# Kernel tuning notes

Hardware: AMD Instinct MI355X
Metric: run time of the kernel (lower is better)

The kernel has to match this reference:

```python
import jax, jax.numpy as jnp
import numpy as np

KH, KW = 3, 3
STRIDE = (1, 1)
PADDING = (1, 1)
DILATION = (1, 1)


def setup_inputs() -> dict:
    key = jax.random.key(0)
    k1, k2, k3, k4, k5 = jax.random.split(key, 5)
    B, Cin, H, W = 8, 64, 128, 128
    Cout = 64
    Ho, Wo = 128, 128  # stride 1, pad 1, k=3 -> same spatial size
    K = KH * KW
    return {
        "input": jax.random.normal(k1, (B, Cin, H, W), dtype=jnp.float32),
        "offset": jax.random.normal(k2, (B, 2 * K, Ho, Wo), dtype=jnp.float32),
        "mask": jax.random.uniform(k3, (B, K, Ho, Wo), dtype=jnp.float32),
        "weight": jax.random.normal(k4, (Cout, Cin, KH, KW), dtype=jnp.float32) * 0.05,
        "bias": jax.random.normal(k5, (Cout,), dtype=jnp.float32) * 0.05,
    }


def _deform_conv2d(x, weight, offset, mask, bias, stride, padding, dilation):
    B, Cin, H, W = x.shape
    Cout, Cing, kh, kw = weight.shape
    G = Cin // Cing                      # weight groups
    K = kh * kw
    Goff = offset.shape[1] // (2 * K)    # offset groups
    Ho, Wo = offset.shape[2], offset.shape[3]
    Cg = Cin // Goff                     # channels per offset group
    sh, sw = stride
    ph, pw = padding
    dh, dw = dilation

    # offsets laid out as (y, x) pairs per kernel tap per offset group
    off = offset.reshape(B, Goff, K, 2, Ho, Wo)
    ky = (jnp.arange(K) // kw).astype(jnp.float32) * dh   # [K]
    kx = (jnp.arange(K) % kw).astype(jnp.float32) * dw
    gy = (jnp.arange(Ho).astype(jnp.float32) * sh - ph)    # [Ho]
    gx = (jnp.arange(Wo).astype(jnp.float32) * sw - pw)
    # sampling positions: [B, Goff, K, Ho, Wo]
    py = off[:, :, :, 0] + ky[None, None, :, None, None] + gy[None, None, None, :, None]
    px = off[:, :, :, 1] + kx[None, None, :, None, None] + gx[None, None, None, None, :]

    y0 = jnp.floor(py)
    x0 = jnp.floor(px)
    ly = py - y0
    lx = px - x0
    y0i = y0.astype(jnp.int32)
    x0i = x0.astype(jnp.int32)

    x_g = x.reshape(B, Goff, Cg, H * W)

    def gather(yi, xi):
        # zero padding outside the image
        valid = (yi >= 0) & (yi < H) & (xi >= 0) & (xi < W)
        yc = jnp.clip(yi, 0, H - 1)
        xc = jnp.clip(xi, 0, W - 1)
        idx = (yc * W + xc).reshape(B, Goff, K * Ho * Wo)
        v = jnp.take_along_axis(x_g, idx[:, :, None, :], axis=3)  # [B,Goff,Cg,K*Ho*Wo]
        return v * valid.reshape(B, Goff, 1, K * Ho * Wo)

    w00 = ((1 - ly) * (1 - lx)).reshape(B, Goff, 1, K * Ho * Wo)
    w01 = ((1 - ly) * lx).reshape(B, Goff, 1, K * Ho * Wo)
    w10 = (ly * (1 - lx)).reshape(B, Goff, 1, K * Ho * Wo)
    w11 = (ly * lx).reshape(B, Goff, 1, K * Ho * Wo)

    sampled = w00 * gather(y0i, x0i)
    sampled = sampled + w01 * gather(y0i, x0i + 1)
    sampled = sampled + w10 * gather(y0i + 1, x0i)
    sampled = sampled + w11 * gather(y0i + 1, x0i + 1)
    sampled = sampled.reshape(B, Goff, Cg, K, Ho, Wo)

    if mask is not None:
        sampled = sampled * mask.reshape(B, Goff, 1, K, Ho, Wo)

    # grouped conv accumulate
    sampled = sampled.reshape(B, G, Cing, K, Ho, Wo)
    w = weight.reshape(G, Cout // G, Cing, K)
    out = jnp.einsum('gock,bgcksq->bgosq', w, sampled).reshape(B, Cout, Ho, Wo)
    if bias is not None:
        out = out + bias[None, :, None, None]
    return out


def reference(input, offset, mask, weight, bias):
    return _deform_conv2d(input, weight, offset, mask, bias, STRIDE, PADDING, DILATION)
```

## Files before the change

kernel.cpp:

```cpp
#include <hip/hip_runtime.h>
#include <hip/hip_fp16.h>

#define HH 128
#define WW 128
#define HW (HH*WW)
#define XT_BYTES ((size_t)8 * HW * 64 * 2)
#define WT_BYTES ((size_t)9 * 2 * 4 * 64 * 8 * 2)

typedef __attribute__((ext_vector_type(8))) short short8;
typedef __attribute__((ext_vector_type(4))) float f32x4;

static __device__ __forceinline__ unsigned short f2bf(float f) {
    unsigned int u = __float_as_uint(f);
    u += 0x7fffu + ((u >> 16) & 1u);
    return (unsigned short)(u >> 16);
}
static __device__ __forceinline__ float bf2f(unsigned short h) {
    return __uint_as_float((unsigned int)h << 16);
}
static __device__ __forceinline__ float blo(unsigned int u) {
    return __uint_as_float(u << 16);
}
static __device__ __forceinline__ float bhi(unsigned int u) {
    return __uint_as_float(u & 0xffff0000u);
}

__global__ void wtrans_kernel(const float* __restrict__ w, unsigned short* __restrict__ wt) {
    int i = blockIdx.x * 256 + threadIdx.x;
    if (i < 9 * 2 * 4 * 64 * 8) {
        int e  = i & 7;
        int l  = (i >> 3) & 63;
        int wv = (i >> 9) & 3;
        int kf = (i >> 11) & 1;
        int k  = i >> 12;
        int co = wv * 16 + (l & 15);
        int c  = kf * 32 + (l >> 4) * 8 + e;
        wt[i] = f2bf(w[(co * 64 + c) * 9 + k]);
    }
}

__global__ __launch_bounds__(256) void xtrans_kernel(const float* __restrict__ x,
                                                     unsigned int* __restrict__ xt32) {
    __shared__ float tile[64][65];
    const int bid = blockIdx.x;
    const int b   = bid >> 8;
    const int hw0 = (bid & 255) << 6;
    const int t   = threadIdx.x;
    #pragma unroll
    for (int i = 0; i < 16; ++i) {
        int idx = (i << 8) + t;
        int c = idx >> 6, j = idx & 63;
        tile[c][j] = x[(size_t)(((b << 6) + c) << 14) + hw0 + j];
    }
    __syncthreads();
    #pragma unroll
    for (int i = 0; i < 8; ++i) {
        int idx = (i << 8) + t;
        int cp = idx & 31, hw = idx >> 5;
        unsigned u = (unsigned)f2bf(tile[2 * cp][hw]) | ((unsigned)f2bf(tile[2 * cp + 1][hw]) << 16);
        xt32[((size_t)((b << 14) + hw0 + hw) << 5) + cp] = u;
    }
}

__global__ __launch_bounds__(256, 5) void deform_nhwc(
    const unsigned short* __restrict__ xt,
    const float* __restrict__ off,
    const float* __restrict__ msk,
    const unsigned short* __restrict__ wt,
    const float* __restrict__ bias,
    float* __restrict__ out)
{
    __shared__ __align__(16) unsigned char smem[30208];
    int4*  moS = (int4*)(smem + 16384);
    uint2* mwH = (uint2*)(smem + 25600);

    const int t   = threadIdx.x;
    const int bid = blockIdx.x;
    const int b   = bid & 7;
    const int rem = bid >> 3;
    const int ho  = rem >> 1;
    const int wo0 = (rem & 1) << 6;
    const int l   = t & 63;
    const int wv_id = __builtin_amdgcn_readfirstlane(t >> 6);

    short8 wtf[2][2];
    #pragma unroll
    for (int kf = 0; kf < 2; ++kf)
        wtf[0][kf] = *(const short8*)(wt + (((kf * 4 + wv_id) * 64 + l) << 3));

    for (int i = t; i < 9 * 64; i += 256) {
        int p = i & 63;
        int k = i >> 6;
        int wo = wo0 + p;
        int obase = ((b * 18 + 2 * k) * HH + ho) * WW + wo;
        float oy = off[obase];
        float ox = off[obase + HW];
        float m  = msk[((b * 9 + k) * HH + ho) * WW + wo];
        float py = oy + (float)(k / 3) + (float)(ho - 1);
        float px = ox + (float)(k % 3) + (float)(wo - 1);
        float fy = floorf(py), fx = floorf(px);
        float ly = py - fy,    lx = px - fx;
        int y0 = (int)fy, x0 = (int)fx;
        int y1 = y0 + 1,  x1 = x0 + 1;
        float vy0 = (y0 >= 0 && y0 < HH) ? 1.f : 0.f;
        float vy1 = (y1 >= 0 && y1 < HH) ? 1.f : 0.f;
        float vx0 = (x0 >= 0 && x0 < WW) ? 1.f : 0.f;
        float vx1 = (x1 >= 0 && x1 < WW) ? 1.f : 0.f;
        float w00 = (1.f - ly) * (1.f - lx) * m * vy0 * vx0;
        float w01 = (1.f - ly) * lx         * m * vy0 * vx1;
        float w10 = ly         * (1.f - lx) * m * vy1 * vx0;
        float w11 = ly         * lx         * m * vy1 * vx1;
        int yc0 = min(max(y0, 0), HH - 1), yc1 = min(max(y1, 0), HH - 1);
        int xc0 = min(max(x0, 0), WW - 1), xc1 = min(max(x1, 0), WW - 1);
        moS[i] = make_int4((yc0 * WW + xc0) << 7, (yc0 * WW + xc1) << 7,
                           (yc1 * WW + xc0) << 7, (yc1 * WW + xc1) << 7);
        __half2 hA = __floats2half2_rn(w00, w01);
        __half2 hB = __floats2half2_rn(w10, w11);
        mwH[i] = make_uint2(*(unsigned int*)&hA, *(unsigned int*)&hB);
    }

    const char* ib = (const char*)xt + (size_t)b * HW * 128;
    const int chb  = (l & 7) << 4;
    const int px0_ = (wv_id << 4) + (l >> 3);
    int st_woff[2];
    st_woff[0] = px0_ * 128 + (chb ^ ((px0_ & 7) << 4));
    st_woff[1] = st_woff[0] + 8 * 128;
    const int lq = (l >> 4) << 4;
    const int sw = (l & 7) << 4;

    __syncthreads();

    auto sample_tap = [&](int k, unsigned char* dst) {
        #pragma unroll
        for (int r = 0; r < 2; ++r) {
            const int px = px0_ + (r << 3);
            int4   ob = moS[k * 64 + px];
            uint2  wp = mwH[k * 64 + px];
            float2 wA = __half22float2(*(const __half2*)&wp.x);
            float2 wB = __half22float2(*(const __half2*)&wp.y);
            uint4 c00 = *(const uint4*)(ib + (ob.x + chb));
            uint4 c01 = *(const uint4*)(ib + (ob.y + chb));
            uint4 c10 = *(const uint4*)(ib + (ob.z + chb));
            uint4 c11 = *(const uint4*)(ib + (ob.w + chb));
            uint4 uv;
            #define CMB(dst_, a0, a1, a2, a3) {                                         \
                float vlo = wA.x*blo(a0) + wA.y*blo(a1) + wB.x*blo(a2) + wB.y*blo(a3);  \
                float vhi = wA.x*bhi(a0) + wA.y*bhi(a1) + wB.x*bhi(a2) + wB.y*bhi(a3);  \
                dst_ = __builtin_amdgcn_perm(__float_as_uint(vhi) + 0x8000u,            \
                                             __float_as_uint(vlo) + 0x8000u, 0x07060302u); }
            CMB(uv.x, c00.x, c01.x, c10.x, c11.x);
            CMB(uv.y, c00.y, c01.y, c10.y, c11.y);
            CMB(uv.z, c00.z, c01.z, c10.z, c11.z);
            CMB(uv.w, c00.w, c01.w, c10.w, c11.w);
            #undef CMB
            *(uint4*)(dst + st_woff[r]) = uv;
        }
    };

    sample_tap(0, smem);
    __syncthreads();

    f32x4 acc[4];
    #pragma unroll
    for (int g = 0; g < 4; ++g) acc[g] = (f32x4){0.f, 0.f, 0.f, 0.f};

    #pragma unroll
    for (int s = 0; s < 9; ++s) {
        if (s < 8) {
            const int kn = s + 1;
            #pragma unroll
            for (int kf = 0; kf < 2; ++kf)
                wtf[kn & 1][kf] = *(const short8*)(wt + ((((kn * 2 + kf) * 4 + wv_id) * 64 + l) << 3));
            sample_tap(kn, smem + ((kn & 1) << 13));
        }
        const unsigned char* rb = smem + ((s & 1) << 13);
        #pragma unroll
        for (int g = 0; g < 4; ++g) {
            const int prow = g * 16 + (l & 15);
            short8 a0 = *(const short8*)(rb + prow * 128 + (lq ^ sw));
            short8 a1 = *(const short8*)(rb + prow * 128 + ((64 + lq) ^ sw));
            acc[g] = __builtin_amdgcn_mfma_f32_16x16x32_bf16(a0, wtf[s & 1][0], acc[g], 0, 0, 0);
            acc[g] = __builtin_amdgcn_mfma_f32_16x16x32_bf16(a1, wtf[s & 1][1], acc[g], 0, 0, 0);
        }
        __syncthreads();
    }

    float* out_t = (float*)smem;
    const int co_e = (wv_id << 4) + (l & 15);
    const float bv = bias[co_e];
    const int swE = (co_e & 15) << 4;
    #pragma unroll
    for (int g = 0; g < 4; ++g) {
        int pxb = (g << 6) + ((l >> 4) << 4);
        float4 v = make_float4(acc[g][0] + bv, acc[g][1] + bv, acc[g][2] + bv, acc[g][3] + bv);
        *(float4*)((unsigned char*)out_t + co_e * 256 + (pxb ^ swE)) = v;
    }
    __syncthreads();
    float* outb = out + (size_t)b * 64 * HW + (size_t)ho * WW + wo0;
    #pragma unroll
    for (int j = 0; j < 4; ++j) {
        int co   = (t >> 4) + (j << 4);
        int colb = (t & 15) << 4;
        float4 v = *(const float4*)((const unsigned char*)out_t + co * 256 + (colb ^ ((co & 15) << 4)));
        *(float4*)&outb[(size_t)co * HW + ((t & 15) << 2)] = v;
    }
}

__global__ __launch_bounds__(256, 4) void deform_fallback(
    const float* __restrict__ x, const float* __restrict__ off,
    const float* __restrict__ msk, const float* __restrict__ wraw,
    const float* __restrict__ bias, float* __restrict__ out)
{
    __shared__ unsigned short s_tile[2][64][68];
    __shared__ __align__(16) unsigned char meta_mem[18432];
    float4* mwS = (float4*)meta_mem;
    int4*   moS = (int4*)(meta_mem + 9216);
    float*  out_t = (float*)meta_mem;

    const int t   = threadIdx.x;
    const int bid = blockIdx.x;
    const int b   = bid & 7;
    const int rem = bid >> 3;
    const int ho  = rem >> 1;
    const int wo0 = (rem & 1) << 6;
    const int l   = t & 63;
    const int wv_id = __builtin_amdgcn_readfirstlane(t >> 6);
    const int c0  = wv_id << 4;
    const int cb  = wv_id << 4;

    short8 wtf[2][2];
    #pragma unroll
    for (int kf = 0; kf < 2; ++kf) {
        short8 f;
        int co = cb + (l & 15);
        int cbase = kf * 32 + (l >> 4) * 8;
        #pragma unroll
        for (int e = 0; e < 8; ++e) f[e] = (short)f2bf(wraw[(co * 64 + cbase + e) * 9 + 0]);
        wtf[0][kf] = f;
    }

    for (int i = t; i < 9 * 64; i += 256) {
        int p = i & 63;
        int k = i >> 6;
        int wo = wo0 + p;
        int obase = ((b * 18 + 2 * k) * HH + ho) * WW + wo;
        float oy = off[obase];
        float ox = off[obase + HW];
        float m  = msk[((b * 9 + k) * HH + ho) * WW + wo];
        float py = oy + (float)(k / 3) + (float)(ho - 1);
        float px = ox + (float)(k % 3) + (float)(wo - 1);
        float fy = floorf(py), fx = floorf(px);
        float ly = py - fy,    lx = px - fx;
        int y0 = (int)fy, x0 = (int)fx;
        int y1 = y0 + 1,  x1 = x0 + 1;
        float vy0 = (y0 >= 0 && y0 < HH) ? 1.f : 0.f;
        float vy1 = (y1 >= 0 && y1 < HH) ? 1.f : 0.f;
        float vx0 = (x0 >= 0 && x0 < WW) ? 1.f : 0.f;
        float vx1 = (x1 >= 0 && x1 < WW) ? 1.f : 0.f;
        float w00 = (1.f - ly) * (1.f - lx) * m * vy0 * vx0;
        float w01 = (1.f - ly) * lx         * m * vy0 * vx1;
        float w10 = ly         * (1.f - lx) * m * vy1 * vx0;
        float w11 = ly         * lx         * m * vy1 * vx1;
        int yc0 = min(max(y0, 0), HH - 1), yc1 = min(max(y1, 0), HH - 1);
        int xc0 = min(max(x0, 0), WW - 1), xc1 = min(max(x1, 0), WW - 1);
        mwS[i] = make_float4(w00, w01, w10, w11);
        moS[i] = make_int4(yc0 * WW + xc0, yc0 * WW + xc1,
                           yc1 * WW + xc0, yc1 * WW + xc1);
    }

    const int p = t & 63;
    const float* xb = x + (size_t)(b * 64 + c0) * HW;
    __syncthreads();

    {
        float4 wv = mwS[p];
        int4   ov = moS[p];
        const float* pc = xb;
        #pragma unroll
        for (int i = 0; i < 16; i += 4) {
            float v0 = wv.x * pc[ov.x] + wv.y * pc[ov.y] + wv.z * pc[ov.z] + wv.w * pc[ov.w]; pc += HW;
            float v1 = wv.x * pc[ov.x] + wv.y * pc[ov.y] + wv.z * pc[ov.z] + wv.w * pc[ov.w]; pc += HW;
            float v2 = wv.x * pc[ov.x] + wv.y * pc[ov.y] + wv.z * pc[ov.z] + wv.w * pc[ov.w]; pc += HW;
            float v3 = wv.x * pc[ov.x] + wv.y * pc[ov.y] + wv.z * pc[ov.z] + wv.w * pc[ov.w]; pc += HW;
            uint2 u;
            u.x = (unsigned)f2bf(v0) | ((unsigned)f2bf(v1) << 16);
            u.y = (unsigned)f2bf(v2) | ((unsigned)f2bf(v3) << 16);
            *(uint2*)&s_tile[0][p][c0 + i] = u;
        }
    }
    __syncthreads();

    f32x4 acc[4];
    #pragma unroll
    for (int g = 0; g < 4; ++g) acc[g] = (f32x4){0.f, 0.f, 0.f, 0.f};

    #pragma unroll
    for (int s = 0; s < 9; ++s) {
        if (s < 8) {
            const int kn = s + 1;
            #pragma unroll
            for (int kf = 0; kf < 2; ++kf) {
                short8 f;
                int co = cb + (l & 15);
                int cbase = kf * 32 + (l >> 4) * 8;
                #pragma unroll
                for (int e = 0; e < 8; ++e) f[e] = (short)f2bf(wraw[(co * 64 + cbase + e) * 9 + kn]);
                wtf[kn & 1][kf] = f;
            }
            float4 wv = mwS[kn * 64 + p];
            int4   ov = moS[kn * 64 + p];
            const float* pc = xb;
            #pragma unroll
            for (int i = 0; i < 16; i += 4) {
                float v0 = wv.x * pc[ov.x] + wv.y * pc[ov.y] + wv.z * pc[ov.z] + wv.w * pc[ov.w]; pc += HW;
                float v1 = wv.x * pc[ov.x] + wv.y * pc[ov.y] + wv.z * pc[ov.z] + wv.w * pc[ov.w]; pc += HW;
                float v2 = wv.x * pc[ov.x] + wv.y * pc[ov.y] + wv.z * pc[ov.z] + wv.w * pc[ov.w]; pc += HW;
                float v3 = wv.x * pc[ov.x] + wv.y * pc[ov.y] + wv.z * pc[ov.z] + wv.w * pc[ov.w]; pc += HW;
                uint2 u;
                u.x = (unsigned)f2bf(v0) | ((unsigned)f2bf(v1) << 16);
                u.y = (unsigned)f2bf(v2) | ((unsigned)f2bf(v3) << 16);
                *(uint2*)&s_tile[kn & 1][p][c0 + i] = u;
            }
        }
        #pragma unroll
        for (int g = 0; g < 4; ++g) {
            const int prow = g * 16 + (l & 15);
            const unsigned short* rp = &s_tile[s & 1][prow][(l >> 4) * 8];
            union { short8 v; unsigned long long q[2]; } ua0, ua1;
            ua0.q[0] = *(const unsigned long long*)(rp);
            ua0.q[1] = *(const unsigned long long*)(rp + 4);
            ua1.q[0] = *(const unsigned long long*)(rp + 32);
            ua1.q[1] = *(const unsigned long long*)(rp + 36);
            acc[g] = __builtin_amdgcn_mfma_f32_16x16x32_bf16(ua0.v, wtf[s & 1][0], acc[g], 0, 0, 0);
            acc[g] = __builtin_amdgcn_mfma_f32_16x16x32_bf16(ua1.v, wtf[s & 1][1], acc[g], 0, 0, 0);
        }
        __syncthreads();
    }

    const float bv = bias[cb + (l & 15)];
    #pragma unroll
    for (int g = 0; g < 4; ++g) {
        int co = cb + (l & 15);
        int pxb = g * 16 + (l >> 4) * 4;
        #pragma unroll
        for (int r = 0; r < 4; ++r)
            out_t[co * 68 + pxb + r] = acc[g][r] + bv;
    }
    __syncthreads();
    float* outb = out + (size_t)b * 64 * HW + (size_t)ho * WW + wo0;
    #pragma unroll
    for (int j = 0; j < 4; ++j) {
        int co  = (t >> 4) + j * 16;
        int px0 = (t & 15) << 2;
        float4 v = *(float4*)&out_t[co * 68 + px0];
        *(float4*)&outb[(size_t)co * HW + px0] = v;
    }
}

extern "C" void kernel_launch(void* const* d_in, const int* in_sizes, int n_in,
                              void* d_out, int out_size, void* d_ws, size_t ws_size,
                              hipStream_t stream) {
    const float* x    = (const float*)d_in[0];
    const float* off  = (const float*)d_in[1];
    const float* msk  = (const float*)d_in[2];
    const float* w    = (const float*)d_in[3];
    const float* bias = (const float*)d_in[4];
    float* out = (float*)d_out;

    const size_t need = XT_BYTES + WT_BYTES;
    if (d_ws != nullptr && ws_size >= need) {
        unsigned int*   xt32 = (unsigned int*)d_ws;
        unsigned short* wt   = (unsigned short*)((char*)d_ws + XT_BYTES);
        xtrans_kernel<<<2048, 256, 0, stream>>>(x, xt32);
        wtrans_kernel<<<144, 256, 0, stream>>>(w, wt);
        deform_nhwc<<<2048, 256, 0, stream>>>((const unsigned short*)xt32, off, msk, wt, bias, out);
    } else {
        deform_fallback<<<2048, 256, 0, stream>>>(x, off, msk, w, bias, out);
    }
}
```

Before: 52.73 us.

## Feed bilinear samples straight into MFMA registers, dropping LDS staging and barriers

Restructures the main loop so each wave samples its own 16 pixels across all 64 channels and builds MFMA A-fragments directly in registers, instead of writing sampled taps to LDS and reading them back. Gathers for the next tap are issued into a double-buffered register set while the current tap is combined, and the per-tap __syncthreads is removed. Each wave now computes all 64 output channels, so it loads 8 weight fragments per tap. Occupancy is lowered to 3 blocks per SM to make room for the larger register footprint, which may reduce the latency hiding available for the gathers.

```diff
diff --git a/kernel.cpp b/kernel.cpp
--- a/kernel.cpp
+++ b/kernel.cpp
@@ -14,9 +14,6 @@
     unsigned int u = __float_as_uint(f);
     u += 0x7fffu + ((u >> 16) & 1u);
     return (unsigned short)(u >> 16);
-}
-static __device__ __forceinline__ float bf2f(unsigned short h) {
-    return __uint_as_float((unsigned int)h << 16);
 }
 static __device__ __forceinline__ float blo(unsigned int u) {
     return __uint_as_float(u << 16);
@@ -62,7 +59,7 @@
     }
 }
 
-__global__ __launch_bounds__(256, 5) void deform_nhwc(
+__global__ __launch_bounds__(256, 3) void deform_nhwc(
     const unsigned short* __restrict__ xt,
     const float* __restrict__ off,
     const float* __restrict__ msk,
@@ -81,12 +78,7 @@
     const int ho  = rem >> 1;
     const int wo0 = (rem & 1) << 6;
     const int l   = t & 63;
-    const int wv_id = __builtin_amdgcn_readfirstlane(t >> 6);
-
-    short8 wtf[2][2];
-    #pragma unroll
-    for (int kf = 0; kf < 2; ++kf)
-        wtf[0][kf] = *(const short8*)(wt + (((kf * 4 + wv_id) * 64 + l) << 3));
+    const int wv  = __builtin_amdgcn_readfirstlane(t >> 6);
 
     for (int i = t; i < 9 * 64; i += 256) {
         int p = i & 63;
@@ -119,80 +111,85 @@
         mwH[i] = make_uint2(*(unsigned int*)&hA, *(unsigned int*)&hB);
     }
 
-    const char* ib = (const char*)xt + (size_t)b * HW * 128;
-    const int chb  = (l & 7) << 4;
-    const int px0_ = (wv_id << 4) + (l >> 3);
-    int st_woff[2];
-    st_woff[0] = px0_ * 128 + (chb ^ ((px0_ & 7) << 4));
-    st_woff[1] = st_woff[0] + 8 * 128;
-    const int lq = (l >> 4) << 4;
-    const int sw = (l & 7) << 4;
-
-    __syncthreads();
-
-    auto sample_tap = [&](int k, unsigned char* dst) {
-        #pragma unroll
-        for (int r = 0; r < 2; ++r) {
-            const int px = px0_ + (r << 3);
-            int4   ob = moS[k * 64 + px];
-            uint2  wp = mwH[k * 64 + px];
-            float2 wA = __half22float2(*(const __half2*)&wp.x);
-            float2 wB = __half22float2(*(const __half2*)&wp.y);
-            uint4 c00 = *(const uint4*)(ib + (ob.x + chb));
-            uint4 c01 = *(const uint4*)(ib + (ob.y + chb));
-            uint4 c10 = *(const uint4*)(ib + (ob.z + chb));
-            uint4 c11 = *(const uint4*)(ib + (ob.w + chb));
-            uint4 uv;
-            #define CMB(dst_, a0, a1, a2, a3) {                                         \
-                float vlo = wA.x*blo(a0) + wA.y*blo(a1) + wB.x*blo(a2) + wB.y*blo(a3);  \
-                float vhi = wA.x*bhi(a0) + wA.y*bhi(a1) + wB.x*bhi(a2) + wB.y*bhi(a3);  \
-                dst_ = __builtin_amdgcn_perm(__float_as_uint(vhi) + 0x8000u,            \
-                                             __float_as_uint(vlo) + 0x8000u, 0x07060302u); }
-            CMB(uv.x, c00.x, c01.x, c10.x, c11.x);
-            CMB(uv.y, c00.y, c01.y, c10.y, c11.y);
-            CMB(uv.z, c00.z, c01.z, c10.z, c11.z);
-            CMB(uv.w, c00.w, c01.w, c10.w, c11.w);
-            #undef CMB
-            *(uint4*)(dst + st_woff[r]) = uv;
+    const char* ib  = (const char*)xt + (size_t)b * HW * 128;
+    const int   px  = (wv << 4) + (l & 15);
+    const int   chb = (l >> 4) << 4;
+
+    __syncthreads();
+
+    f32x4 acc[4];
+    #pragma unroll
+    for (int g = 0; g < 4; ++g) acc[g] = (f32x4){0.f, 0.f, 0.f, 0.f};
+
+    uint4 ga[8], gb[8];
+
+    #define ISSUE_G(g, kk) {                                                \
+        int4 ob = moS[(kk) * 64 + px];                                      \
+        g[0] = *(const uint4*)(ib + ob.x + chb);                            \
+        g[1] = *(const uint4*)(ib + ob.x + chb + 64);                       \
+        g[2] = *(const uint4*)(ib + ob.y + chb);                            \
+        g[3] = *(const uint4*)(ib + ob.y + chb + 64);                       \
+        g[4] = *(const uint4*)(ib + ob.z + chb);                            \
+        g[5] = *(const uint4*)(ib + ob.z + chb + 64);                       \
+        g[6] = *(const uint4*)(ib + ob.w + chb);                            \
+        g[7] = *(const uint4*)(ib + ob.w + chb + 64);                       \
+    }
+
+    #define CMB(dst_, a0, a1, a2, a3) {                                     \
+        float vlo = wA.x*blo(a0) + wA.y*blo(a1) + wB.x*blo(a2) + wB.y*blo(a3); \
+        float vhi = wA.x*bhi(a0) + wA.y*bhi(a1) + wB.x*bhi(a2) + wB.y*bhi(a3); \
+        dst_ = __builtin_amdgcn_perm(__float_as_uint(vhi) + 0x8000u,        \
+                                     __float_as_uint(vlo) + 0x8000u, 0x07060302u); }
+
+    #define COMBINE_MFMA(g, kk, bfr) {                                      \
+        uint2 wp = mwH[(kk) * 64 + px];                                     \
+        float2 wA = __half22float2(*(const __half2*)&wp.x);                 \
+        float2 wB = __half22float2(*(const __half2*)&wp.y);                 \
+        short8 af[2];                                                       \
+        _Pragma("unroll")                                                   \
+        for (int kf = 0; kf < 2; ++kf) {                                    \
+            uint4 c00 = g[0 + kf], c01 = g[2 + kf], c10 = g[4 + kf], c11 = g[6 + kf]; \
+            unsigned r0, r1, r2, r3;                                        \
+            CMB(r0, c00.x, c01.x, c10.x, c11.x);                            \
+            CMB(r1, c00.y, c01.y, c10.y, c11.y);                            \
+            CMB(r2, c00.z, c01.z, c10.z, c11.z);                            \
+            CMB(r3, c00.w, c01.w, c10.w, c11.w);                            \
+            union { unsigned u[4]; short8 s; } uu = {{r0, r1, r2, r3}};     \
+            af[kf] = uu.s;                                                  \
+        }                                                                   \
+        _Pragma("unroll")                                                   \
+        for (int cot = 0; cot < 4; ++cot) {                                 \
+            acc[cot] = __builtin_amdgcn_mfma_f32_16x16x32_bf16(af[0], bfr[cot],     acc[cot], 0, 0, 0); \
+            acc[cot] = __builtin_amdgcn_mfma_f32_16x16x32_bf16(af[1], bfr[4 + cot], acc[cot], 0, 0, 0); \
+        }                                                                   \
+    }
+
+    ISSUE_G(ga, 0)
+
+    #pragma unroll
+    for (int k = 0; k < 9; ++k) {
+        short8 bfr[8];
+        #pragma unroll
+        for (int q = 0; q < 8; ++q)
+            bfr[q] = *(const short8*)(wt + (((k * 8 + q) * 64 + l) << 3));
+        if (k < 8) {
+            if (k & 1) { ISSUE_G(ga, k + 1) } else { ISSUE_G(gb, k + 1) }
         }
-    };
-
-    sample_tap(0, smem);
-    __syncthreads();
-
-    f32x4 acc[4];
-    #pragma unroll
-    for (int g = 0; g < 4; ++g) acc[g] = (f32x4){0.f, 0.f, 0.f, 0.f};
-
-    #pragma unroll
-    for (int s = 0; s < 9; ++s) {
-        if (s < 8) {
-            const int kn = s + 1;
-            #pragma unroll
-            for (int kf = 0; kf < 2; ++kf)
-                wtf[kn & 1][kf] = *(const short8*)(wt + ((((kn * 2 + kf) * 4 + wv_id) * 64 + l) << 3));
-            sample_tap(kn, smem + ((kn & 1) << 13));
-        }
-        const unsigned char* rb = smem + ((s & 1) << 13);
-        #pragma unroll
-        for (int g = 0; g < 4; ++g) {
-            const int prow = g * 16 + (l & 15);
-            short8 a0 = *(const short8*)(rb + prow * 128 + (lq ^ sw));
-            short8 a1 = *(const short8*)(rb + prow * 128 + ((64 + lq) ^ sw));
-            acc[g] = __builtin_amdgcn_mfma_f32_16x16x32_bf16(a0, wtf[s & 1][0], acc[g], 0, 0, 0);
-            acc[g] = __builtin_amdgcn_mfma_f32_16x16x32_bf16(a1, wtf[s & 1][1], acc[g], 0, 0, 0);
-        }
-        __syncthreads();
-    }
+        if (k & 1) { COMBINE_MFMA(gb, k, bfr) } else { COMBINE_MFMA(ga, k, bfr) }
+    }
+    #undef ISSUE_G
+    #undef CMB
+    #undef COMBINE_MFMA
 
     float* out_t = (float*)smem;
-    const int co_e = (wv_id << 4) + (l & 15);
-    const float bv = bias[co_e];
-    const int swE = (co_e & 15) << 4;
-    #pragma unroll
-    for (int g = 0; g < 4; ++g) {
-        int pxb = (g << 6) + ((l >> 4) << 4);
-        float4 v = make_float4(acc[g][0] + bv, acc[g][1] + bv, acc[g][2] + bv, acc[g][3] + bv);
+    const int pxb = (wv << 6) + ((l >> 4) << 4);
+    const int swE = (l & 15) << 4;
+    #pragma unroll
+    for (int cot = 0; cot < 4; ++cot) {
+        int co_e = (cot << 4) + (l & 15);
+        float bv = bias[co_e];
+        float4 v = make_float4(acc[cot][0] + bv, acc[cot][1] + bv,
+                               acc[cot][2] + bv, acc[cot][3] + bv);
         *(float4*)((unsigned char*)out_t + co_e * 256 + (pxb ^ swE)) = v;
     }
     __syncthreads();
```

Measured after the change: 97.31 us. +84.6%, slower.

## Issue next-tap gathers before MFMA and combine after to overlap latency

Applied to the files above, without the earlier changes.

Splits the per-tap bilinear sampling into a gather-issue phase and a combine/store phase. The global loads for the next tap are issued before the current tap's MFMA block, and the blend runs afterwards, with sched_barriers keeping the compiler from reordering them. The blend math now uses packed two-float vector ops, and launch bounds drop from 5 to 4 blocks per CU to leave room for the extra live registers. The aim is to hide gather latency behind the matrix work, at the cost of register pressure and lower occupancy.

```diff
diff --git a/kernel.cpp b/kernel.cpp
--- a/kernel.cpp
+++ b/kernel.cpp
@@ -9,21 +9,20 @@
 
 typedef __attribute__((ext_vector_type(8))) short short8;
 typedef __attribute__((ext_vector_type(4))) float f32x4;
+typedef __attribute__((ext_vector_type(2))) float f32x2;
 
 static __device__ __forceinline__ unsigned short f2bf(float f) {
     unsigned int u = __float_as_uint(f);
     u += 0x7fffu + ((u >> 16) & 1u);
     return (unsigned short)(u >> 16);
 }
-static __device__ __forceinline__ float bf2f(unsigned short h) {
-    return __uint_as_float((unsigned int)h << 16);
-}
-static __device__ __forceinline__ float blo(unsigned int u) {
-    return __uint_as_float(u << 16);
-}
-static __device__ __forceinline__ float bhi(unsigned int u) {
-    return __uint_as_float(u & 0xffff0000u);
-}
+static __device__ __forceinline__ f32x2 ub2(unsigned u) {
+    f32x2 r;
+    r.x = __uint_as_float(u << 16);
+    r.y = __uint_as_float(u & 0xffff0000u);
+    return r;
+}
+static __device__ __forceinline__ f32x2 spl(float f) { f32x2 r; r.x = f; r.y = f; return r; }
 
 __global__ void wtrans_kernel(const float* __restrict__ w, unsigned short* __restrict__ wt) {
     int i = blockIdx.x * 256 + threadIdx.x;
@@ -62,7 +61,7 @@
     }
 }
 
-__global__ __launch_bounds__(256, 5) void deform_nhwc(
+__global__ __launch_bounds__(256, 4) void deform_nhwc(
     const unsigned short* __restrict__ xt,
     const float* __restrict__ off,
     const float* __restrict__ msk,
@@ -81,12 +80,7 @@
     const int ho  = rem >> 1;
     const int wo0 = (rem & 1) << 6;
     const int l   = t & 63;
-    const int wv_id = __builtin_amdgcn_readfirstlane(t >> 6);
-
-    short8 wtf[2][2];
-    #pragma unroll
-    for (int kf = 0; kf < 2; ++kf)
-        wtf[0][kf] = *(const short8*)(wt + (((kf * 4 + wv_id) * 64 + l) << 3));
+    const int wv  = __builtin_amdgcn_readfirstlane(t >> 6);
 
     for (int i = t; i < 9 * 64; i += 256) {
         int p = i & 63;
@@ -119,45 +113,70 @@
         mwH[i] = make_uint2(*(unsigned int*)&hA, *(unsigned int*)&hB);
     }
 
-    const char* ib = (const char*)xt + (size_t)b * HW * 128;
-    const int chb  = (l & 7) << 4;
-    const int px0_ = (wv_id << 4) + (l >> 3);
+    const char* ib   = (const char*)xt + (size_t)b * HW * 128;
+    const int  chb   = (l & 7) << 4;
+    const int  px0_  = (wv << 4) + (l >> 3);
     int st_woff[2];
     st_woff[0] = px0_ * 128 + (chb ^ ((px0_ & 7) << 4));
     st_woff[1] = st_woff[0] + 8 * 128;
     const int lq = (l >> 4) << 4;
     const int sw = (l & 7) << 4;
 
-    __syncthreads();
-
-    auto sample_tap = [&](int k, unsigned char* dst) {
-        #pragma unroll
-        for (int r = 0; r < 2; ++r) {
-            const int px = px0_ + (r << 3);
-            int4   ob = moS[k * 64 + px];
-            uint2  wp = mwH[k * 64 + px];
-            float2 wA = __half22float2(*(const __half2*)&wp.x);
-            float2 wB = __half22float2(*(const __half2*)&wp.y);
-            uint4 c00 = *(const uint4*)(ib + (ob.x + chb));
-            uint4 c01 = *(const uint4*)(ib + (ob.y + chb));
-            uint4 c10 = *(const uint4*)(ib + (ob.z + chb));
-            uint4 c11 = *(const uint4*)(ib + (ob.w + chb));
-            uint4 uv;
-            #define CMB(dst_, a0, a1, a2, a3) {                                         \
-                float vlo = wA.x*blo(a0) + wA.y*blo(a1) + wB.x*blo(a2) + wB.y*blo(a3);  \
-                float vhi = wA.x*bhi(a0) + wA.y*bhi(a1) + wB.x*bhi(a2) + wB.y*bhi(a3);  \
-                dst_ = __builtin_amdgcn_perm(__float_as_uint(vhi) + 0x8000u,            \
-                                             __float_as_uint(vlo) + 0x8000u, 0x07060302u); }
-            CMB(uv.x, c00.x, c01.x, c10.x, c11.x);
-            CMB(uv.y, c00.y, c01.y, c10.y, c11.y);
-            CMB(uv.z, c00.z, c01.z, c10.z, c11.z);
-            CMB(uv.w, c00.w, c01.w, c10.w, c11.w);
-            #undef CMB
-            *(uint4*)(dst + st_woff[r]) = uv;
-        }
-    };
-
-    sample_tap(0, smem);
+    uint4  g0[4], g1[4];
+    short8 wtf[2][2];
+
+    #define ISSUE_TAP(kk) {                                          \
+        int4 ob0 = moS[(kk) * 64 + px0_];                            \
+        g0[0] = *(const uint4*)(ib + ob0.x + chb);                   \
+        g0[1] = *(const uint4*)(ib + ob0.y + chb);                   \
+        g0[2] = *(const uint4*)(ib + ob0.z + chb);                   \
+        g0[3] = *(const uint4*)(ib + ob0.w + chb);                   \
+        int4 ob1 = moS[(kk) * 64 + px0_ + 8];                        \
+        g1[0] = *(const uint4*)(ib + ob1.x + chb);                   \
+        g1[1] = *(const uint4*)(ib + ob1.y + chb);                   \
+        g1[2] = *(const uint4*)(ib + ob1.z + chb);                   \
+        g1[3] = *(const uint4*)(ib + ob1.w + chb);                   \
+    }
+
+    #define CMB_V(dst_, c00, c01, c10, c11) {                        \
+        f32x2 v = spl(wA.x) * ub2(c00) + spl(wA.y) * ub2(c01)        \
+                + spl(wB.x) * ub2(c10) + spl(wB.y) * ub2(c11);       \
+        dst_ = __builtin_amdgcn_perm(__float_as_uint(v.y) + 0x8000u, \
+                                     __float_as_uint(v.x) + 0x8000u, 0x07060302u); \
+    }
+
+    #define COMBINE_STORE(kk, dstb) {                                \
+        {                                                            \
+            uint2 wp = mwH[(kk) * 64 + px0_];                        \
+            float2 wA = __half22float2(*(const __half2*)&wp.x);      \
+            float2 wB = __half22float2(*(const __half2*)&wp.y);      \
+            uint4 uv;                                                \
+            CMB_V(uv.x, g0[0].x, g0[1].x, g0[2].x, g0[3].x)          \
+            CMB_V(uv.y, g0[0].y, g0[1].y, g0[2].y, g0[3].y)          \
+            CMB_V(uv.z, g0[0].z, g0[1].z, g0[2].z, g0[3].z)          \
+            CMB_V(uv.w, g0[0].w, g0[1].w, g0[2].w, g0[3].w)          \
+            *(uint4*)((dstb) + st_woff[0]) = uv;                     \
+        }                                                            \
+        {                                                            \
+            uint2 wp = mwH[(kk) * 64 + px0_ + 8];                    \
+            float2 wA = __half22float2(*(const __half2*)&wp.x);      \
+            float2 wB = __half22float2(*(const __half2*)&wp.y);      \
+            uint4 uv;                                                \
+            CMB_V(uv.x, g1[0].x, g1[1].x, g1[2].x, g1[3].x)          \
+            CMB_V(uv.y, g1[0].y, g1[1].y, g1[2].y, g1[3].y)          \
+            CMB_V(uv.z, g1[0].z, g1[1].z, g1[2].z, g1[3].z)          \
+            CMB_V(uv.w, g1[0].w, g1[1].w, g1[2].w, g1[3].w)          \
+            *(uint4*)((dstb) + st_woff[1]) = uv;                     \
+        }                                                            \
+    }
+
+    __syncthreads();
+
+    ISSUE_TAP(0)
+    #pragma unroll
+    for (int kf = 0; kf < 2; ++kf)
+        wtf[0][kf] = *(const short8*)(wt + (((kf * 4 + wv) * 64 + l) << 3));
+    COMBINE_STORE(0, smem)
     __syncthreads();
 
     f32x4 acc[4];
@@ -168,25 +187,36 @@
     for (int s = 0; s < 9; ++s) {
         if (s < 8) {
             const int kn = s + 1;
+            ISSUE_TAP(kn)
             #pragma unroll
             for (int kf = 0; kf < 2; ++kf)
-                wtf[kn & 1][kf] = *(const short8*)(wt + ((((kn * 2 + kf) * 4 + wv_id) * 64 + l) << 3));
-            sample_tap(kn, smem + ((kn & 1) << 13));
-        }
-        const unsigned char* rb = smem + ((s & 1) << 13);
-        #pragma unroll
-        for (int g = 0; g < 4; ++g) {
-            const int prow = g * 16 + (l & 15);
-            short8 a0 = *(const short8*)(rb + prow * 128 + (lq ^ sw));
-            short8 a1 = *(const short8*)(rb + prow * 128 + ((64 + lq) ^ sw));
-            acc[g] = __builtin_amdgcn_mfma_f32_16x16x32_bf16(a0, wtf[s & 1][0], acc[g], 0, 0, 0);
-            acc[g] = __builtin_amdgcn_mfma_f32_16x16x32_bf16(a1, wtf[s & 1][1], acc[g], 0, 0, 0);
+                wtf[kn & 1][kf] = *(const short8*)(wt + ((((kn * 2 + kf) * 4 + wv) * 64 + l) << 3));
+        }
+        __builtin_amdgcn_sched_barrier(0);
+        {
+            const unsigned char* rb = smem + ((s & 1) << 13);
+            #pragma unroll
+            for (int g = 0; g < 4; ++g) {
+                const int prow = g * 16 + (l & 15);
+                short8 a0 = *(const short8*)(rb + prow * 128 + (lq ^ sw));
+                short8 a1 = *(const short8*)(rb + prow * 128 + ((64 + lq) ^ sw));
+                acc[g] = __builtin_amdgcn_mfma_f32_16x16x32_bf16(a0, wtf[s & 1][0], acc[g], 0, 0, 0);
+                acc[g] = __builtin_amdgcn_mfma_f32_16x16x32_bf16(a1, wtf[s & 1][1], acc[g], 0, 0, 0);
+            }
+        }
+        __builtin_amdgcn_sched_barrier(0);
+        if (s < 8) {
+            COMBINE_STORE(s + 1, smem + (((s + 1) & 1) << 13))
         }
         __syncthreads();
     }
+    #undef ISSUE_TAP
+    #undef CMB_V
+    #undef COMBINE_STORE
 
     float* out_t = (float*)smem;
-    const int co_e = (wv_id << 4) + (l & 15);
+    const int cb = wv << 4;
+    const int co_e = cb + (l & 15);
     const float bv = bias[co_e];
     const int swE = (co_e & 15) << 4;
     #pragma unroll
```

Measured after the change: 52.36 us. About the same (-0.7%).
